# Optimization experiments

Hardware: AMD Instinct MI355X
Metric: run time of the kernel (lower is better)

## Reference

```python
import jax, jax.numpy as jnp
import numpy as np

N_NODES = 50000
N_EDGES = 800000
HIDDEN = 128
NUM_GDL = 2


def setup_inputs() -> dict:
    key = jax.random.key(0)
    k0, k1, k2, k3, k4 = jax.random.split(key, 5)
    x = jax.random.normal(k0, (N_NODES, HIDDEN), dtype=jnp.float32)
    row = jax.random.randint(k1, (N_EDGES,), 0, N_NODES, dtype=jnp.int32)
    # ensure every node appears at least once as a target so degree >= 1
    col_tail = jax.random.randint(k2, (N_EDGES - N_NODES,), 0, N_NODES, dtype=jnp.int32)
    col = jnp.concatenate([jnp.arange(N_NODES, dtype=jnp.int32), col_tail])
    edge_index = jnp.stack([row, col], axis=0)  # [2, E]
    W1s = jax.random.normal(k3, (NUM_GDL, HIDDEN, HIDDEN), dtype=jnp.float32) / np.sqrt(HIDDEN).astype(np.float32)
    W2s = jax.random.normal(k4, (NUM_GDL, HIDDEN, 2 * HIDDEN), dtype=jnp.float32) / np.sqrt(2 * HIDDEN).astype(np.float32)
    biases = jnp.zeros((NUM_GDL, HIDDEN), dtype=jnp.float32)  # reset_parameters zeroes bias
    return {"x": x, "edge_index": edge_index, "W1s": W1s, "W2s": W2s, "biases": biases}


def reference(x, edge_index, W1s, W2s, biases):
    # eval mode: dropout is identity
    row, col = edge_index[0], edge_index[1]  # row = source j, col = target i
    n, d = x.shape
    deg = jax.ops.segment_sum(jnp.ones(row.shape[0], x.dtype), col, num_segments=n)
    norm = (1.0 / deg)[row]  # per-edge norm, indexed by row as in torch source
    for k in range(W1s.shape[0]):
        W1, W2, b = W1s[k], W2s[k], biases[k]
        # lin2(cat[x_i, x_j]) = x_i @ W2[:, :d].T + x_j @ W2[:, d:].T
        # precompute both node-level projections, then gather per edge (cheaper than per-edge GEMM)
        proj_i = x @ W2[:, :d].T  # [n, d]
        proj_j = x @ W2[:, d:].T  # [n, d]
        msg = norm[:, None] * (proj_i[col] + proj_j[row])  # [E, d]
        agg = jax.ops.segment_sum(msg, col, num_segments=n)  # scatter-add into targets
        out = x @ W1.T - agg + b
        x = jax.nn.gelu(out, approximate=False)  # torch nn.GELU default = exact erf
    return x
```

## Files before the change

### kernel.cpp

```cpp
#include <hip/hip_runtime.h>

#define N_NODES 50000
#define N_EDGES 800000
#define D 128
#define NBUCKET 196
#define CAP 8192
#define EPT 16
#define SCAT_BLOCKS 196
#define WCONV_BLOCKS 96
#define GEMM_TILES 391

typedef unsigned short ushort_t;
typedef __bf16 bf16x8 __attribute__((ext_vector_type(8)));
typedef float f32x4 __attribute__((ext_vector_type(4)));
typedef float f32x2 __attribute__((ext_vector_type(2)));

__device__ __forceinline__ ushort_t f2bf(float f) {
    unsigned u = __builtin_bit_cast(unsigned, f);
    u += 0x7FFFu + ((u >> 16) & 1u);
    return (ushort_t)(u >> 16);
}
__device__ __forceinline__ float bf2f(unsigned h16) {
    return __builtin_bit_cast(float, h16 << 16);
}

__global__ __launch_bounds__(256) void k_pre(const int* __restrict__ row, const int* __restrict__ col,
                                             int* __restrict__ bucket_cursor, unsigned* __restrict__ temp,
                                             const float* __restrict__ W1s, const float* __restrict__ W2s,
                                             ushort_t* __restrict__ Wb) {
    __shared__ int hist[NBUCKET];
    int b = blockIdx.x;
    if (b < SCAT_BLOCKS) {
        for (int t = threadIdx.x; t < NBUCKET; t += 256) hist[t] = 0;
        __syncthreads();
        int base = (b * 256 + threadIdx.x) * EPT;
        bool act = base < N_EDGES;
        int4 c[4], r[4];
        if (act) {
            #pragma unroll
            for (int q = 0; q < 4; ++q) c[q] = *(const int4*)(col + base + q * 4);
            #pragma unroll
            for (int q = 0; q < 4; ++q) r[q] = *(const int4*)(row + base + q * 4);
            #pragma unroll
            for (int q = 0; q < 4; ++q) {
                atomicAdd(&hist[c[q].x >> 8], 1); atomicAdd(&hist[c[q].y >> 8], 1);
                atomicAdd(&hist[c[q].z >> 8], 1); atomicAdd(&hist[c[q].w >> 8], 1);
            }
        }
        __syncthreads();
        for (int t = threadIdx.x; t < NBUCKET; t += 256) {
            int cnt = hist[t];
            hist[t] = cnt ? atomicAdd(&bucket_cursor[t], cnt) : 0;
        }
        __syncthreads();
        if (act) {
            #pragma unroll
            for (int q = 0; q < 4; ++q) {
                int cc[4] = { c[q].x, c[q].y, c[q].z, c[q].w };
                int rr[4] = { r[q].x, r[q].y, r[q].z, r[q].w };
                #pragma unroll
                for (int e = 0; e < 4; ++e) {
                    int bk = cc[e] >> 8;
                    int pos = atomicAdd(&hist[bk], 1);
                    temp[bk * CAP + pos] = (unsigned)rr[e] | ((unsigned)(cc[e] & 255) << 16);
                }
            }
        }
    } else {
        int c = (b - SCAT_BLOCKS) * 256 + threadIdx.x;
        int k = c / 12288, rem = c % 12288;
        int mat = rem / 4096, rr = (rem % 4096) / 32, col4 = rem % 32;
        const float* src = (mat == 0)
            ? (W1s + k * 16384 + rr * 128 + col4 * 4)
            : (W2s + k * 32768 + rr * 256 + (mat == 2 ? 128 : 0) + col4 * 4);
        float4 v = *(const float4*)src;
        ushort_t tmp[4] = { f2bf(v.x), f2bf(v.y), f2bf(v.z), f2bf(v.w) };
        *(uint2*)(Wb + ((size_t)(k * 3 + mat)) * 16384 + rr * 128 + col4 * 4) = *(const uint2*)tmp;
    }
}

template<bool AF32>
__device__ __forceinline__ void gemm_tile3(int m0, ushort_t (*As)[136],
                                           const void* __restrict__ xsrc,
                                           const ushort_t* __restrict__ Wl,
                                           const float* __restrict__ scl,
                                           ushort_t* __restrict__ Plb,
                                           ushort_t* __restrict__ Pi_,
                                           unsigned char* __restrict__ Pj8) {
    const int tid = threadIdx.x;
    if constexpr (AF32) {
        const float* xf = (const float*)xsrc;
        #pragma unroll
        for (int it = 0; it < 8; ++it) {
            int c = tid + it * 256;
            int r = c >> 4, kc = c & 15;
            uint4 v = make_uint4(0, 0, 0, 0);
            int gm = m0 + r;
            if (gm < N_NODES) {
                float4 p0 = *(const float4*)(xf + (size_t)gm * D + kc * 8);
                float4 p1 = *(const float4*)(xf + (size_t)gm * D + kc * 8 + 4);
                ushort_t __attribute__((aligned(16))) tmp[8] =
                    { f2bf(p0.x), f2bf(p0.y), f2bf(p0.z), f2bf(p0.w),
                      f2bf(p1.x), f2bf(p1.y), f2bf(p1.z), f2bf(p1.w) };
                v = *(const uint4*)tmp;
            }
            *(uint4*)&As[r][kc * 8] = v;
        }
    } else {
        const ushort_t* xb = (const ushort_t*)xsrc;
        #pragma unroll
        for (int it = 0; it < 8; ++it) {
            int c = tid + it * 256;
            int r = c >> 4, kc = c & 15;
            uint4 v = make_uint4(0, 0, 0, 0);
            int gm = m0 + r;
            if (gm < N_NODES) v = *(const uint4*)(xb + (size_t)gm * D + kc * 8);
            *(uint4*)&As[r][kc * 8] = v;
        }
    }
    __syncthreads();
    const int w = tid >> 6, lane = tid & 63, quad = lane >> 4, r16 = lane & 15;
    const int arow0 = w * 32 + r16, arow1 = arow0 + 16;
    #pragma unroll
    for (int y = 0; y < 3; ++y) {
        const ushort_t* Wmat = Wl + (size_t)y * 16384;
        f32x4 acc[2][8];
        #pragma unroll
        for (int mt = 0; mt < 2; ++mt)
            #pragma unroll
            for (int nt = 0; nt < 8; ++nt) acc[mt][nt] = (f32x4){0.f, 0.f, 0.f, 0.f};
        #pragma unroll
        for (int k0 = 0; k0 < 128; k0 += 32) {
            bf16x8 a0 = __builtin_bit_cast(bf16x8, *(const uint4*)&As[arow0][k0 + quad * 8]);
            bf16x8 a1 = __builtin_bit_cast(bf16x8, *(const uint4*)&As[arow1][k0 + quad * 8]);
            #pragma unroll
            for (int nt = 0; nt < 8; ++nt) {
                bf16x8 b = __builtin_bit_cast(bf16x8,
                    *(const uint4*)(Wmat + (nt * 16 + r16) * 128 + k0 + quad * 8));
                acc[0][nt] = __builtin_amdgcn_mfma_f32_16x16x32_bf16(b, a0, acc[0][nt], 0, 0, 0);
                acc[1][nt] = __builtin_amdgcn_mfma_f32_16x16x32_bf16(b, a1, acc[1][nt], 0, 0, 0);
            }
        }
        #pragma unroll
        for (int mt = 0; mt < 2; ++mt) {
            int gm = m0 + w * 32 + mt * 16 + r16;
            if (gm >= N_NODES) continue;
            if (y < 2) {
                ushort_t* Outp = (y == 0) ? Plb : Pi_;
                #pragma unroll
                for (int nt = 0; nt < 8; ++nt) {
                    ushort_t tmp[4] = { f2bf(acc[mt][nt][0]), f2bf(acc[mt][nt][1]),
                                        f2bf(acc[mt][nt][2]), f2bf(acc[mt][nt][3]) };
                    *(uint2*)(Outp + (size_t)gm * D + nt * 16 + quad * 4) = *(const uint2*)tmp;
                }
            } else {
                float sc = scl ? scl[gm] : 1.0f;
                #pragma unroll
                for (int nt = 0; nt < 8; ++nt) {
                    int v = __builtin_amdgcn_cvt_pk_fp8_f32(acc[mt][nt][0] * sc, acc[mt][nt][1] * sc, 0, false);
                    v = __builtin_amdgcn_cvt_pk_fp8_f32(acc[mt][nt][2] * sc, acc[mt][nt][3] * sc, v, true);
                    *(unsigned*)(Pj8 + (size_t)gm * D + nt * 16 + quad * 4) = (unsigned)v;
                }
            }
        }
    }
}

union __align__(16) LdsBG {
    ushort_t As[128][136];
    struct { int hist[256]; int sm[256]; } s;
};

__global__ __launch_bounds__(256, 4) void k_bsort_gemm(const unsigned* __restrict__ temp,
                                                       const int* __restrict__ bucket_cursor,
                                                       ushort_t* __restrict__ csr, int* __restrict__ off,
                                                       int* __restrict__ deg, float* __restrict__ inv_deg,
                                                       const float* __restrict__ xf,
                                                       const ushort_t* __restrict__ Wb,
                                                       ushort_t* __restrict__ Plb,
                                                       ushort_t* __restrict__ Pi_,
                                                       unsigned char* __restrict__ Pj8) {
    __shared__ LdsBG lds;
    if (blockIdx.x < NBUCKET) {
        int* hist = lds.s.hist;
        int* sm = lds.s.sm;
        int b = blockIdx.x, t = threadIdx.x;
        int cnt = bucket_cursor[b];
        sm[t] = (t < b) ? bucket_cursor[t] : 0;
        __syncthreads();
        for (int o = 1; o < 256; o <<= 1) {
            int add = (t >= o) ? sm[t - o] : 0;
            __syncthreads();
            sm[t] += add;
            __syncthreads();
        }
        int gbase = sm[255];
        int tbase = b * CAP;
        hist[t] = 0;
        __syncthreads();
        int i = t;
        for (; i + 768 < cnt; i += 1024) {
            unsigned e0 = temp[tbase + i], e1 = temp[tbase + i + 256];
            unsigned e2 = temp[tbase + i + 512], e3 = temp[tbase + i + 768];
            atomicAdd(&hist[e0 >> 16], 1); atomicAdd(&hist[e1 >> 16], 1);
            atomicAdd(&hist[e2 >> 16], 1); atomicAdd(&hist[e3 >> 16], 1);
        }
        for (; i < cnt; i += 256) atomicAdd(&hist[temp[tbase + i] >> 16], 1);
        __syncthreads();
        int c = hist[t];
        sm[t] = c;
        __syncthreads();
        for (int o = 1; o < 256; o <<= 1) {
            int add = (t >= o) ? sm[t - o] : 0;
            __syncthreads();
            sm[t] += add;
            __syncthreads();
        }
        int excl = sm[t] - c;
        int node = b * 256 + t;
        if (node < N_NODES) {
            off[node] = gbase + excl;
            deg[node] = c;
            inv_deg[node] = 1.0f / (float)c;
        }
        __syncthreads();
        hist[t] = gbase + excl;
        __syncthreads();
        i = t;
        for (; i + 768 < cnt; i += 1024) {
            unsigned e0 = temp[tbase + i], e1 = temp[tbase + i + 256];
            unsigned e2 = temp[tbase + i + 512], e3 = temp[tbase + i + 768];
            int p0 = atomicAdd(&hist[e0 >> 16], 1);
            int p1 = atomicAdd(&hist[e1 >> 16], 1);
            int p2 = atomicAdd(&hist[e2 >> 16], 1);
            int p3 = atomicAdd(&hist[e3 >> 16], 1);
            csr[p0] = (ushort_t)e0; csr[p1] = (ushort_t)e1;
            csr[p2] = (ushort_t)e2; csr[p3] = (ushort_t)e3;
        }
        for (; i < cnt; i += 256) {
            unsigned e = temp[tbase + i];
            int p = atomicAdd(&hist[e >> 16], 1);
            csr[p] = (ushort_t)e;
        }
    } else {
        gemm_tile3<true>((blockIdx.x - NBUCKET) * 128, lds.As, xf, Wb, nullptr, Plb, Pi_, Pj8);
    }
}

__global__ __launch_bounds__(256, 4) void k_gemm(const ushort_t* __restrict__ xb,
                                                 const ushort_t* __restrict__ Wl,
                                                 const float* __restrict__ inv_deg,
                                                 ushort_t* __restrict__ Plb,
                                                 ushort_t* __restrict__ Pi_,
                                                 unsigned char* __restrict__ Pj8) {
    __shared__ __align__(16) ushort_t As[128][136];
    gemm_tile3<false>(blockIdx.x * 128, As, xb, Wl, inv_deg, Plb, Pi_, Pj8);
}

__global__ __launch_bounds__(256, 8) void k_agg(const ushort_t* __restrict__ Plb,
                                                const ushort_t* __restrict__ Pi_,
                                                const unsigned char* __restrict__ Pj8,
                                                const int* __restrict__ off,
                                                const int* __restrict__ deg,
                                                const ushort_t* __restrict__ csr,
                                                const float* __restrict__ inv_deg,
                                                const float* __restrict__ bias,
                                                float* __restrict__ s_arr,
                                                float* __restrict__ out_f32,
                                                ushort_t* __restrict__ out_bf16,
                                                int layer0) {
    int wv = __builtin_amdgcn_readfirstlane(threadIdx.x >> 6);
    int node = blockIdx.x * 4 + wv;
    if (node >= N_NODES) return;
    const int lane = threadIdx.x & 63;
    const int g = lane >> 4;
    const int q8 = lane & 15;
    const int eoff = 8 * q8 + 2 * g;
    unsigned ulin = *(const unsigned*)(Plb + (size_t)node * D + eoff);
    unsigned upi  = *(const unsigned*)(Pi_ + (size_t)node * D + eoff);
    float2 bv = *(const float2*)(bias + eoff);
    float su[8];
    #pragma unroll
    for (int k = 0; k < 8; ++k) su[k] = 0.f;
    float sd = 0.f;
    const int e0 = off[node], ne = deg[node];
    int j = 0;
    if (layer0) {
        for (; j + 16 <= ne; j += 16) {
            int sx[4];
            #pragma unroll
            for (int t = 0; t < 4; ++t) sx[t] = csr[e0 + j + 4 * t + g];
            uint2 uu[4];
            #pragma unroll
            for (int t = 0; t < 4; ++t) uu[t] = *(const uint2*)(Pj8 + (size_t)sx[t] * D + 8 * q8);
            float dv[4];
            #pragma unroll
            for (int t = 0; t < 4; ++t) dv[t] = inv_deg[sx[t]];
            #pragma unroll
            for (int t = 0; t < 4; ++t) {
                f32x2 f0 = __builtin_amdgcn_cvt_pk_f32_fp8((int)uu[t].x, false);
                f32x2 f1 = __builtin_amdgcn_cvt_pk_f32_fp8((int)uu[t].x, true);
                f32x2 f2 = __builtin_amdgcn_cvt_pk_f32_fp8((int)uu[t].y, false);
                f32x2 f3 = __builtin_amdgcn_cvt_pk_f32_fp8((int)uu[t].y, true);
                sd += dv[t];
                su[0] += dv[t] * f0[0]; su[1] += dv[t] * f0[1];
                su[2] += dv[t] * f1[0]; su[3] += dv[t] * f1[1];
                su[4] += dv[t] * f2[0]; su[5] += dv[t] * f2[1];
                su[6] += dv[t] * f3[0]; su[7] += dv[t] * f3[1];
            }
        }
        for (; j + 4 <= ne; j += 4) {
            int sx = csr[e0 + j + g];
            uint2 uu = *(const uint2*)(Pj8 + (size_t)sx * D + 8 * q8);
            float dv = inv_deg[sx];
            f32x2 f0 = __builtin_amdgcn_cvt_pk_f32_fp8((int)uu.x, false);
            f32x2 f1 = __builtin_amdgcn_cvt_pk_f32_fp8((int)uu.x, true);
            f32x2 f2 = __builtin_amdgcn_cvt_pk_f32_fp8((int)uu.y, false);
            f32x2 f3 = __builtin_amdgcn_cvt_pk_f32_fp8((int)uu.y, true);
            sd += dv;
            su[0] += dv * f0[0]; su[1] += dv * f0[1];
            su[2] += dv * f1[0]; su[3] += dv * f1[1];
            su[4] += dv * f2[0]; su[5] += dv * f2[1];
            su[6] += dv * f3[0]; su[7] += dv * f3[1];
        }
        if (j < ne) {
            int r = ne - j;
            int gi = (g < r) ? g : (r - 1);
            int sx = csr[e0 + j + gi];
            uint2 uu = *(const uint2*)(Pj8 + (size_t)sx * D + 8 * q8);
            float dv = (g < r) ? inv_deg[sx] : 0.f;
            f32x2 f0 = __builtin_amdgcn_cvt_pk_f32_fp8((int)uu.x, false);
            f32x2 f1 = __builtin_amdgcn_cvt_pk_f32_fp8((int)uu.x, true);
            f32x2 f2 = __builtin_amdgcn_cvt_pk_f32_fp8((int)uu.y, false);
            f32x2 f3 = __builtin_amdgcn_cvt_pk_f32_fp8((int)uu.y, true);
            sd += dv;
            su[0] += dv * f0[0]; su[1] += dv * f0[1];
            su[2] += dv * f1[0]; su[3] += dv * f1[1];
            su[4] += dv * f2[0]; su[5] += dv * f2[1];
            su[6] += dv * f3[0]; su[7] += dv * f3[1];
        }
    } else {
        for (; j + 16 <= ne; j += 16) {
            int sx[4];
            #pragma unroll
            for (int t = 0; t < 4; ++t) sx[t] = csr[e0 + j + 4 * t + g];
            uint2 uu[4];
            #pragma unroll
            for (int t = 0; t < 4; ++t) uu[t] = *(const uint2*)(Pj8 + (size_t)sx[t] * D + 8 * q8);
            #pragma unroll
            for (int t = 0; t < 4; ++t) {
                f32x2 f0 = __builtin_amdgcn_cvt_pk_f32_fp8((int)uu[t].x, false);
                f32x2 f1 = __builtin_amdgcn_cvt_pk_f32_fp8((int)uu[t].x, true);
                f32x2 f2 = __builtin_amdgcn_cvt_pk_f32_fp8((int)uu[t].y, false);
                f32x2 f3 = __builtin_amdgcn_cvt_pk_f32_fp8((int)uu[t].y, true);
                su[0] += f0[0]; su[1] += f0[1];
                su[2] += f1[0]; su[3] += f1[1];
                su[4] += f2[0]; su[5] += f2[1];
                su[6] += f3[0]; su[7] += f3[1];
            }
        }
        for (; j + 4 <= ne; j += 4) {
            int sx = csr[e0 + j + g];
            uint2 uu = *(const uint2*)(Pj8 + (size_t)sx * D + 8 * q8);
            f32x2 f0 = __builtin_amdgcn_cvt_pk_f32_fp8((int)uu.x, false);
            f32x2 f1 = __builtin_amdgcn_cvt_pk_f32_fp8((int)uu.x, true);
            f32x2 f2 = __builtin_amdgcn_cvt_pk_f32_fp8((int)uu.y, false);
            f32x2 f3 = __builtin_amdgcn_cvt_pk_f32_fp8((int)uu.y, true);
            su[0] += f0[0]; su[1] += f0[1];
            su[2] += f1[0]; su[3] += f1[1];
            su[4] += f2[0]; su[5] += f2[1];
            su[6] += f3[0]; su[7] += f3[1];
        }
        if (j < ne) {
            int r = ne - j;
            int gi = (g < r) ? g : (r - 1);
            int sx = csr[e0 + j + gi];
            uint2 uu = *(const uint2*)(Pj8 + (size_t)sx * D + 8 * q8);
            float wt = (g < r) ? 1.f : 0.f;
            f32x2 f0 = __builtin_amdgcn_cvt_pk_f32_fp8((int)uu.x, false);
            f32x2 f1 = __builtin_amdgcn_cvt_pk_f32_fp8((int)uu.x, true);
            f32x2 f2 = __builtin_amdgcn_cvt_pk_f32_fp8((int)uu.y, false);
            f32x2 f3 = __builtin_amdgcn_cvt_pk_f32_fp8((int)uu.y, true);
            su[0] += wt * f0[0]; su[1] += wt * f0[1];
            su[2] += wt * f1[0]; su[3] += wt * f1[1];
            su[4] += wt * f2[0]; su[5] += wt * f2[1];
            su[6] += wt * f3[0]; su[7] += wt * f3[1];
        }
    }
    #pragma unroll
    for (int k = 0; k < 8; ++k) {
        su[k] += __shfl_xor(su[k], 16);
        su[k] += __shfl_xor(su[k], 32);
    }
    float si;
    if (layer0) {
        sd += __shfl_xor(sd, 16);
        sd += __shfl_xor(sd, 32);
        si = sd;
        if (lane == 0) s_arr[node] = si;
    } else {
        si = s_arr[node];
    }
    float t0 = (g < 2) ? ((g == 0) ? su[0] : su[2]) : ((g == 2) ? su[4] : su[6]);
    float t1 = (g < 2) ? ((g == 0) ? su[1] : su[3]) : ((g == 2) ? su[5] : su[7]);
    float a0 = bf2f(ulin & 0xffffu) + bv.x - si * bf2f(upi & 0xffffu) - t0;
    float a1 = bf2f(ulin >> 16)     + bv.y - si * bf2f(upi >> 16)     - t1;
    float g0 = 0.5f * a0 * (1.0f + erff(a0 * 0.70710678118654752440f));
    float g1 = 0.5f * a1 * (1.0f + erff(a1 * 0.70710678118654752440f));
    if (layer0) {
        ushort_t tmp[2] = { f2bf(g0), f2bf(g1) };
        *(unsigned*)(out_bf16 + (size_t)node * D + eoff) = *(const unsigned*)tmp;
    } else {
        *(float2*)(out_f32 + (size_t)node * D + eoff) = make_float2(g0, g1);
    }
}

extern "C" void kernel_launch(void* const* d_in, const int* in_sizes, int n_in,
                              void* d_out, int out_size, void* d_ws, size_t ws_size,
                              hipStream_t stream) {
    const float* x      = (const float*)d_in[0];
    const int*   ei     = (const int*)d_in[1];
    const int*   rowp   = ei;
    const int*   colp   = ei + N_EDGES;
    const float* W1s    = (const float*)d_in[2];
    const float* W2s    = (const float*)d_in[3];
    const float* biases = (const float*)d_in[4];
    float* out = (float*)d_out;

    char* ws = (char*)d_ws;
    size_t o = 0;
    auto carve = [&](size_t bytes) -> void* {
        void* p = ws + o;
        o = (o + bytes + 255) & ~(size_t)255;
        return p;
    };
    int*           bucket_cursor = (int*)carve(NBUCKET * 4);
    int*           deg     = (int*)carve(N_NODES * 4);
    float*         inv_deg = (float*)carve(N_NODES * 4);
    int*           off     = (int*)carve(N_NODES * 4);
    float*         s_arr   = (float*)carve(N_NODES * 4);
    ushort_t*      csr     = (ushort_t*)carve((size_t)N_EDGES * 2);
    unsigned*      temp    = (unsigned*)carve((size_t)NBUCKET * CAP * 4);
    ushort_t*      xb      = (ushort_t*)carve((size_t)N_NODES * D * 2);
    ushort_t*      Wb      = (ushort_t*)carve((size_t)2 * 3 * 16384 * 2);
    ushort_t*      Plb     = (ushort_t*)carve((size_t)N_NODES * D * 2);
    ushort_t*      Pi_     = (ushort_t*)carve((size_t)N_NODES * D * 2);
    unsigned char* Pj8     = (unsigned char*)carve((size_t)N_NODES * D);
    if (o > ws_size) return;

    hipMemsetAsync(bucket_cursor, 0, NBUCKET * 4, stream);

    k_pre<<<SCAT_BLOCKS + WCONV_BLOCKS, 256, 0, stream>>>(rowp, colp, bucket_cursor, temp,
                                                          W1s, W2s, Wb);
    k_bsort_gemm<<<NBUCKET + GEMM_TILES, 256, 0, stream>>>(temp, bucket_cursor, csr, off,
                                                           deg, inv_deg, x, Wb, Plb, Pi_, Pj8);

    const int AB = (N_NODES + 3) / 4;
    k_agg<<<AB, 256, 0, stream>>>(Plb, Pi_, Pj8, off, deg, csr, inv_deg, biases, s_arr,
                                  nullptr, xb, 1);
    k_gemm<<<GEMM_TILES, 256, 0, stream>>>(xb, Wb + (size_t)3 * 16384, inv_deg, Plb, Pi_, Pj8);
    k_agg<<<AB, 256, 0, stream>>>(Plb, Pi_, Pj8, off, deg, csr, inv_deg, biases + 128, s_arr,
                                  out, nullptr, 0);
}
```

Before: 238.3 us.

## Keep A operand in registers and stage weights in LDS for GEMM

```diff
diff --git a/kernel.cpp b/kernel.cpp
--- a/kernel.cpp
+++ b/kernel.cpp
@@ -23,6 +23,12 @@
 __device__ __forceinline__ float bf2f(unsigned h16) {
     return __builtin_bit_cast(float, h16 << 16);
 }
+__device__ __forceinline__ bf16x8 pack8(float4 p0, float4 p1) {
+    ushort_t __attribute__((aligned(16))) t[8] =
+        { f2bf(p0.x), f2bf(p0.y), f2bf(p0.z), f2bf(p0.w),
+          f2bf(p1.x), f2bf(p1.y), f2bf(p1.z), f2bf(p1.w) };
+    return __builtin_bit_cast(bf16x8, *(const uint4*)t);
+}
 
 __global__ __launch_bounds__(256) void k_pre(const int* __restrict__ row, const int* __restrict__ col,
                                              int* __restrict__ bucket_cursor, unsigned* __restrict__ temp,
@@ -80,7 +86,7 @@
 }
 
 template<bool AF32>
-__device__ __forceinline__ void gemm_tile3(int m0, ushort_t (*As)[136],
+__device__ __forceinline__ void gemm_tile3(int m0, ushort_t (*Bs)[136],
                                            const void* __restrict__ xsrc,
                                            const ushort_t* __restrict__ Wl,
                                            const float* __restrict__ scl,
@@ -88,62 +94,67 @@
                                            ushort_t* __restrict__ Pi_,
                                            unsigned char* __restrict__ Pj8) {
     const int tid = threadIdx.x;
+    const int w = tid >> 6, lane = tid & 63, quad = lane >> 4, r16 = lane & 15;
+    const int gm0 = m0 + w * 32 + r16, gm1 = gm0 + 16;
+    bf16x8 a0[4], a1[4];
     if constexpr (AF32) {
         const float* xf = (const float*)xsrc;
+        #pragma unroll
+        for (int kk = 0; kk < 4; ++kk) {
+            int colc = kk * 32 + quad * 8;
+            float4 p0 = {0.f,0.f,0.f,0.f}, p1 = {0.f,0.f,0.f,0.f};
+            float4 q0 = {0.f,0.f,0.f,0.f}, q1 = {0.f,0.f,0.f,0.f};
+            if (gm0 < N_NODES) {
+                p0 = *(const float4*)(xf + (size_t)gm0 * D + colc);
+                p1 = *(const float4*)(xf + (size_t)gm0 * D + colc + 4);
+            }
+            if (gm1 < N_NODES) {
+                q0 = *(const float4*)(xf + (size_t)gm1 * D + colc);
+                q1 = *(const float4*)(xf + (size_t)gm1 * D + colc + 4);
+            }
+            a0[kk] = pack8(p0, p1);
+            a1[kk] = pack8(q0, q1);
+        }
+    } else {
+        const ushort_t* xb = (const ushort_t*)xsrc;
+        #pragma unroll
+        for (int kk = 0; kk < 4; ++kk) {
+            int colc = kk * 32 + quad * 8;
+            uint4 v0 = make_uint4(0,0,0,0), v1 = make_uint4(0,0,0,0);
+            if (gm0 < N_NODES) v0 = *(const uint4*)(xb + (size_t)gm0 * D + colc);
+            if (gm1 < N_NODES) v1 = *(const uint4*)(xb + (size_t)gm1 * D + colc);
+            a0[kk] = __builtin_bit_cast(bf16x8, v0);
+            a1[kk] = __builtin_bit_cast(bf16x8, v1);
+        }
+    }
+    #pragma unroll
+    for (int y = 0; y < 3; ++y) {
+        const ushort_t* Wmat = Wl + (size_t)y * 16384;
         #pragma unroll
         for (int it = 0; it < 8; ++it) {
             int c = tid + it * 256;
             int r = c >> 4, kc = c & 15;
-            uint4 v = make_uint4(0, 0, 0, 0);
-            int gm = m0 + r;
-            if (gm < N_NODES) {
-                float4 p0 = *(const float4*)(xf + (size_t)gm * D + kc * 8);
-                float4 p1 = *(const float4*)(xf + (size_t)gm * D + kc * 8 + 4);
-                ushort_t __attribute__((aligned(16))) tmp[8] =
-                    { f2bf(p0.x), f2bf(p0.y), f2bf(p0.z), f2bf(p0.w),
-                      f2bf(p1.x), f2bf(p1.y), f2bf(p1.z), f2bf(p1.w) };
-                v = *(const uint4*)tmp;
-            }
-            *(uint4*)&As[r][kc * 8] = v;
-        }
-    } else {
-        const ushort_t* xb = (const ushort_t*)xsrc;
-        #pragma unroll
-        for (int it = 0; it < 8; ++it) {
-            int c = tid + it * 256;
-            int r = c >> 4, kc = c & 15;
-            uint4 v = make_uint4(0, 0, 0, 0);
-            int gm = m0 + r;
-            if (gm < N_NODES) v = *(const uint4*)(xb + (size_t)gm * D + kc * 8);
-            *(uint4*)&As[r][kc * 8] = v;
-        }
-    }
-    __syncthreads();
-    const int w = tid >> 6, lane = tid & 63, quad = lane >> 4, r16 = lane & 15;
-    const int arow0 = w * 32 + r16, arow1 = arow0 + 16;
-    #pragma unroll
-    for (int y = 0; y < 3; ++y) {
-        const ushort_t* Wmat = Wl + (size_t)y * 16384;
+            *(uint4*)&Bs[r][kc * 8] = *(const uint4*)(Wmat + r * 128 + kc * 8);
+        }
+        __syncthreads();
         f32x4 acc[2][8];
         #pragma unroll
         for (int mt = 0; mt < 2; ++mt)
             #pragma unroll
             for (int nt = 0; nt < 8; ++nt) acc[mt][nt] = (f32x4){0.f, 0.f, 0.f, 0.f};
         #pragma unroll
-        for (int k0 = 0; k0 < 128; k0 += 32) {
-            bf16x8 a0 = __builtin_bit_cast(bf16x8, *(const uint4*)&As[arow0][k0 + quad * 8]);
-            bf16x8 a1 = __builtin_bit_cast(bf16x8, *(const uint4*)&As[arow1][k0 + quad * 8]);
+        for (int kk = 0; kk < 4; ++kk) {
             #pragma unroll
             for (int nt = 0; nt < 8; ++nt) {
                 bf16x8 b = __builtin_bit_cast(bf16x8,
-                    *(const uint4*)(Wmat + (nt * 16 + r16) * 128 + k0 + quad * 8));
-                acc[0][nt] = __builtin_amdgcn_mfma_f32_16x16x32_bf16(b, a0, acc[0][nt], 0, 0, 0);
-                acc[1][nt] = __builtin_amdgcn_mfma_f32_16x16x32_bf16(b, a1, acc[1][nt], 0, 0, 0);
+                    *(const uint4*)&Bs[nt * 16 + r16][kk * 32 + quad * 8]);
+                acc[0][nt] = __builtin_amdgcn_mfma_f32_16x16x32_bf16(b, a0[kk], acc[0][nt], 0, 0, 0);
+                acc[1][nt] = __builtin_amdgcn_mfma_f32_16x16x32_bf16(b, a1[kk], acc[1][nt], 0, 0, 0);
             }
         }
         #pragma unroll
         for (int mt = 0; mt < 2; ++mt) {
-            int gm = m0 + w * 32 + mt * 16 + r16;
+            int gm = (mt == 0) ? gm0 : gm1;
             if (gm >= N_NODES) continue;
             if (y < 2) {
                 ushort_t* Outp = (y == 0) ? Plb : Pi_;
@@ -163,11 +174,12 @@
                 }
             }
         }
+        if (y < 2) __syncthreads();
     }
 }
 
 union __align__(16) LdsBG {
-    ushort_t As[128][136];
+    ushort_t Bs[128][136];
     struct { int hist[256]; int sm[256]; } s;
 };
 
@@ -243,7 +255,7 @@
             csr[p] = (ushort_t)e;
         }
     } else {
-        gemm_tile3<true>((blockIdx.x - NBUCKET) * 128, lds.As, xf, Wb, nullptr, Plb, Pi_, Pj8);
+        gemm_tile3<true>((blockIdx.x - NBUCKET) * 128, lds.Bs, xf, Wb, nullptr, Plb, Pi_, Pj8);
     }
 }
 
@@ -253,22 +265,22 @@
                                                  ushort_t* __restrict__ Plb,
                                                  ushort_t* __restrict__ Pi_,
                                                  unsigned char* __restrict__ Pj8) {
-    __shared__ __align__(16) ushort_t As[128][136];
-    gemm_tile3<false>(blockIdx.x * 128, As, xb, Wl, inv_deg, Plb, Pi_, Pj8);
-}
-
-__global__ __launch_bounds__(256, 8) void k_agg(const ushort_t* __restrict__ Plb,
-                                                const ushort_t* __restrict__ Pi_,
-                                                const unsigned char* __restrict__ Pj8,
-                                                const int* __restrict__ off,
-                                                const int* __restrict__ deg,
-                                                const ushort_t* __restrict__ csr,
-                                                const float* __restrict__ inv_deg,
-                                                const float* __restrict__ bias,
-                                                float* __restrict__ s_arr,
-                                                float* __restrict__ out_f32,
-                                                ushort_t* __restrict__ out_bf16,
-                                                int layer0) {
+    __shared__ __align__(16) ushort_t Bs[128][136];
+    gemm_tile3<false>(blockIdx.x * 128, Bs, xb, Wl, inv_deg, Plb, Pi_, Pj8);
+}
+
+__global__ __launch_bounds__(256) void k_agg(const ushort_t* __restrict__ Plb,
+                                             const ushort_t* __restrict__ Pi_,
+                                             const unsigned char* __restrict__ Pj8,
+                                             const int* __restrict__ off,
+                                             const int* __restrict__ deg,
+                                             const ushort_t* __restrict__ csr,
+                                             const float* __restrict__ inv_deg,
+                                             const float* __restrict__ bias,
+                                             float* __restrict__ s_arr,
+                                             float* __restrict__ out_f32,
+                                             ushort_t* __restrict__ out_bf16,
+                                             int layer0) {
     int wv = __builtin_amdgcn_readfirstlane(threadIdx.x >> 6);
     int node = blockIdx.x * 4 + wv;
     if (node >= N_NODES) return;
```

After: 219.9 us. 7.7% less time.
